# Kernel tuning notes

Hardware: AMD Instinct MI355X
Metric: run time of the kernel (lower is better)

Reference implementation:

```python
import jax, jax.numpy as jnp
import numpy as np

T, H, E, I, TOP_K = 4096, 1024, 8, 2048, 2
EPS = 1e-05


def setup_inputs() -> dict:
    key = jax.random.key(0)
    ks = jax.random.split(key, 4)
    x = jax.random.normal(ks[0], (T, H), dtype=jnp.float32)
    scale = jnp.ones((H,), dtype=jnp.float32)
    gate_kernel = jax.random.normal(ks[1], (H, E), dtype=jnp.float32) * (1.0 / np.sqrt(H))
    gate_bias = jnp.zeros((E,), dtype=jnp.float32)
    mlp1_weight = jax.random.normal(ks[2], (E, H, 2 * I), dtype=jnp.float32) * (1.0 / np.sqrt(H))
    mlp1_bias = jnp.zeros((E, 2 * I), dtype=jnp.float32)
    mlp2_weight = jax.random.normal(ks[3], (E, I, H), dtype=jnp.float32) * (1.0 / np.sqrt(I))
    mlp2_bias = jnp.zeros((E, H), dtype=jnp.float32)
    return {"x": x, "scale": scale, "gate_kernel": gate_kernel, "gate_bias": gate_bias,
            "mlp1_weight": mlp1_weight, "mlp1_bias": mlp1_bias,
            "mlp2_weight": mlp2_weight, "mlp2_bias": mlp2_bias}


def _rmsnorm(x, scale):
    t = x.astype(jnp.float32)
    rms = jnp.sqrt(jnp.mean(t * t, axis=-1, keepdims=True) + EPS)
    return ((t / rms) * scale).astype(x.dtype)


def reference(x, scale, gate_kernel, gate_bias, mlp1_weight, mlp1_bias, mlp2_weight, mlp2_bias):
    normed = _rmsnorm(x, scale)                                   # [T, H]
    _ = normed @ gate_kernel + gate_bias                          # gate logits (unused: static routing)
    # dense per-token, all-expert MLP: [T,H] x [E,H,2I] -> [T,E,2I]
    hidden = jnp.einsum('th,ehi->tei', normed, mlp1_weight) + mlp1_bias
    gate = jnp.minimum(hidden[..., :I], 7.0)
    linear = jnp.clip(hidden[..., I:], -7.0, 7.0)
    activated = gate * jax.nn.sigmoid(1.702 * gate) * (linear + 1.0)
    expert_out = jnp.einsum('tei,eih->teh', activated, mlp2_weight) + mlp2_bias  # [T,E,H]
    # static uniform routing over the first TOP_K experts
    mix = jnp.where(jnp.arange(E) < TOP_K, 1.0 / TOP_K, 0.0).astype(x.dtype)     # [E]
    fused = jnp.einsum('teh,e->th', expert_out, mix)
    return x + fused
```

## Files before the change

### kernel.cpp

```cpp
#include <hip/hip_runtime.h>
#include <hip/hip_bf16.h>
#include <stdint.h>

#define T_DIM 4096
#define H_DIM 1024
#define I_DIM 2048

typedef __bf16 bf16x8 __attribute__((ext_vector_type(8)));
typedef float f32x4 __attribute__((ext_vector_type(4)));
typedef unsigned short ushort_t;
typedef unsigned short us4 __attribute__((ext_vector_type(4)));

__device__ __forceinline__ unsigned short f32_to_bf16(float f) {
  unsigned int u = __float_as_uint(f);
  u += 0x7fffu + ((u >> 16) & 1u);
  return (unsigned short)(u >> 16);
}

__device__ __forceinline__ void gload_lds16(const void* g, void* l) {
  __builtin_amdgcn_global_load_lds(
      (__attribute__((address_space(1))) void*)(uintptr_t)g,
      (__attribute__((address_space(3))) void*)(unsigned int)(uintptr_t)l,
      16, 0, 0);
}

__device__ __forceinline__ int swz(int L) { return L ^ (((L >> 7) & 7) << 4); }

#define S_BARRIER() asm volatile("s_barrier" ::: "memory")
#define WAITV(n) asm volatile("s_waitcnt vmcnt(" #n ")" ::: "memory")
#define IRFENCE() asm volatile("" ::: "memory")
#define MFMA16(acc, va, vb) \
  acc = __builtin_amdgcn_mfma_f32_16x16x32_bf16(va, vb, acc, 0, 0, 0)

__device__ __forceinline__ void transpose_body(const float* __restrict__ src,
                                               ushort_t* __restrict__ dst,
                                               int R, int C, int bx, int by,
                                               int bz, float (*tile)[33]) {
  const size_t eoff = (size_t)bz * (size_t)R * (size_t)C;
  src += eoff;
  dst += eoff;
  const int x0 = bx * 32, y0 = by * 32;
  const int tx = threadIdx.x & 31, ty = threadIdx.x >> 5;
#pragma unroll
  for (int i = 0; i < 4; ++i)
    tile[ty + 8 * i][tx] = src[(size_t)(y0 + ty + 8 * i) * C + x0 + tx];
  __syncthreads();
#pragma unroll
  for (int i = 0; i < 4; ++i)
    dst[(size_t)(x0 + ty + 8 * i) * R + y0 + tx] = f32_to_bf16(tile[tx][ty + 8 * i]);
}

__global__ __launch_bounds__(256) void k_prep1(
    const float* __restrict__ x, const float* __restrict__ scale,
    const float* __restrict__ b2, const float* __restrict__ w1,
    ushort_t* __restrict__ normed, float* __restrict__ out,
    ushort_t* __restrict__ w1T) {
  __shared__ __align__(16) float shm[32][33];
  const int bid = blockIdx.x;
  if (bid < T_DIM) {
    const int row = bid, tid = threadIdx.x;
    const float4 v = ((const float4*)(x + (size_t)row * H_DIM))[tid];
    float ss = v.x * v.x + v.y * v.y + v.z * v.z + v.w * v.w;
#pragma unroll
    for (int off = 32; off > 0; off >>= 1) ss += __shfl_xor(ss, off);
    if ((tid & 63) == 0) shm[0][tid >> 6] = ss;
    __syncthreads();
    const float tot = shm[0][0] + shm[0][1] + shm[0][2] + shm[0][3];
    const float inv = rsqrtf(tot * (1.0f / H_DIM) + 1e-5f);
    const float4 sc = ((const float4*)scale)[tid];
    us4 o;
    o.x = f32_to_bf16(v.x * inv * sc.x);
    o.y = f32_to_bf16(v.y * inv * sc.y);
    o.z = f32_to_bf16(v.z * inv * sc.z);
    o.w = f32_to_bf16(v.w * inv * sc.w);
    ((us4*)(normed + (size_t)row * H_DIM))[tid] = o;
    const float4 b0 = ((const float4*)b2)[tid];
    const float4 b1 = ((const float4*)(b2 + H_DIM))[tid];
    float4 ov;
    ov.x = v.x + 0.5f * (b0.x + b1.x);
    ov.y = v.y + 0.5f * (b0.y + b1.y);
    ov.z = v.z + 0.5f * (b0.z + b1.z);
    ov.w = v.w + 0.5f * (b0.w + b1.w);
    ((float4*)(out + (size_t)row * H_DIM))[tid] = ov;
  } else {
    const int t = bid - T_DIM;
    transpose_body(w1, w1T, H_DIM, 2 * I_DIM, t & 127, (t >> 7) & 31, t >> 12,
                   shm);
  }
}

__global__ __launch_bounds__(256, 2) void k_gemm1_tr2(
    const ushort_t* __restrict__ normed, const ushort_t* __restrict__ w1T,
    const float* __restrict__ b1, ushort_t* __restrict__ act,
    const float* __restrict__ w2, ushort_t* __restrict__ w2T) {
  __shared__ __align__(16) ushort_t lds[3][3][4096];
  char* const ldsB = (char*)&lds[0][0][0];
  if (blockIdx.x >= 1024) {
    const int t = blockIdx.x - 1024;
    transpose_body(w2, w2T, I_DIM, H_DIM, t & 31, (t >> 5) & 63, t >> 11,
                   (float(*)[33])ldsB);
    return;
  }
  const int tid = threadIdx.x;
  const int wg = ((blockIdx.x & 7) << 7) + (blockIdx.x >> 3);
  const int e = wg >> 9;
  const int rem = wg & 511;
  const int brow = (rem >> 4) * 128;
  const int bcol = (rem & 15) * 128;
  const int lane = tid & 63;
  const int wid = tid >> 6;
  const int wm = wid >> 1, wn = wid & 1;
  const int r16 = lane & 15, kh = lane >> 4;

  const ushort_t* gBase = w1T + ((size_t)e * 2 * I_DIM + bcol) * H_DIM;
  const ushort_t* lBase = w1T + ((size_t)e * 2 * I_DIM + I_DIM + bcol) * H_DIM;

  f32x4 accg[4][4], accl[4][4];
  const f32x4 zf = {0.f, 0.f, 0.f, 0.f};
#pragma unroll
  for (int m = 0; m < 4; ++m)
#pragma unroll
    for (int n = 0; n < 4; ++n) { accg[m][n] = zf; accl[m][n] = zf; }

  const ushort_t* pA[2];
  const ushort_t* pG[2];
  const ushort_t* pL[2];
#pragma unroll
  for (int j = 0; j < 2; ++j) {
    const int u = swz(j * 4096 + tid * 16);
    const int r = u >> 6, c = (u & 63) >> 1;
    pA[j] = normed + (size_t)(brow + r) * H_DIM + c;
    pG[j] = gBase + (size_t)r * H_DIM + c;
    pL[j] = lBase + (size_t)r * H_DIM + c;
  }
  const int ldst0 = (tid & ~63) * 16;

  const int abase = swz((wm * 64 + r16) * 64 + kh * 16);
  const int bbase = 8192 + swz((wn * 64 + r16) * 64 + kh * 16);

  auto stage = [&](int buf) {
#pragma unroll
    for (int j = 0; j < 2; ++j) {
      gload_lds16(pA[j], ldsB + buf * 24576 + j * 4096 + ldst0);
      gload_lds16(pG[j], ldsB + buf * 24576 + 8192 + j * 4096 + ldst0);
      gload_lds16(pL[j], ldsB + buf * 24576 + 16384 + j * 4096 + ldst0);
    }
  };

  bf16x8 a[4], bg[4], bl[4];

#define G1_ADV()                                                              \
  {                                                                           \
    _Pragma("unroll") for (int j = 0; j < 2; ++j) {                           \
      pA[j] += 32; pG[j] += 32; pL[j] += 32;                                  \
    }                                                                         \
  }
#define G1_RD(C)                                                              \
  _Pragma("unroll") for (int m = 0; m < 4; ++m)                               \
      a[m] = *(const bf16x8*)(ldsB + (C) * 24576 + abase + m * 1024);         \
  _Pragma("unroll") for (int n = 0; n < 4; ++n) {                             \
    bg[n] = *(const bf16x8*)(ldsB + (C) * 24576 + bbase + n * 1024);          \
    bl[n] = *(const bf16x8*)(ldsB + (C) * 24576 + bbase + 8192 + n * 1024);   \
  }
#define G1_MFMA()                                                             \
  _Pragma("unroll") for (int m = 0; m < 4; ++m)                               \
      _Pragma("unroll") for (int n = 0; n < 4; ++n) {                         \
    MFMA16(accg[m][n], a[m], bg[n]);                                          \
    MFMA16(accl[m][n], a[m], bl[n]);                                          \
  }
#define G1_STEP(C, N)                                                         \
  {                                                                           \
    G1_RD(C);                                                                 \
    stage(N);                                                                 \
    __builtin_amdgcn_s_setprio(1);                                            \
    G1_MFMA();                                                                \
    __builtin_amdgcn_s_setprio(0);                                            \
    WAITV(6);                                                                 \
    S_BARRIER();                                                              \
    G1_ADV();                                                                 \
  }

  stage(0); IRFENCE();
  G1_ADV();
  stage(1);
  G1_ADV();
  WAITV(6);
  S_BARRIER();

#pragma unroll 1
  for (int it = 0; it < 10; ++it) {
    G1_STEP(0, 2);
    G1_STEP(1, 0);
    G1_STEP(2, 1);
  }
  {
    G1_RD(0);
    G1_MFMA();
    WAITV(0);
    S_BARRIER();
    G1_RD(1);
    G1_MFMA();
  }
#undef G1_STEP
#undef G1_MFMA
#undef G1_RD
#undef G1_ADV

  const float* b1e = b1 + (size_t)e * 2 * I_DIM;
#pragma unroll
  for (int m = 0; m < 4; ++m)
#pragma unroll
    for (int n = 0; n < 4; ++n) {
      const int gcol = bcol + wn * 64 + n * 16 + r16;
      const float bgb = b1e[gcol];
      const float blb = b1e[I_DIM + gcol];
#pragma unroll
      for (int rr = 0; rr < 4; ++rr) {
        const int grow = brow + wm * 64 + m * 16 + kh * 4 + rr;
        const float hg = accg[m][n][rr] + bgb;
        const float hl = accl[m][n][rr] + blb;
        const float g = fminf(hg, 7.f);
        const float l = fminf(fmaxf(hl, -7.f), 7.f);
        const float s = 1.f / (1.f + __expf(-1.702f * g));
        const float av = g * s * (l + 1.f);
        act[((size_t)e * T_DIM + grow) * I_DIM + gcol] = f32_to_bf16(av);
      }
    }
}

__global__ __launch_bounds__(512, 2) void k_gemm2(
    const ushort_t* __restrict__ act, const ushort_t* __restrict__ w2T,
    float* __restrict__ out) {
  __shared__ __align__(16) ushort_t lds[3][2][8192];
  char* const ldsB = (char*)&lds[0][0][0];
  const int tid = threadIdx.x;
  const int bid = blockIdx.x;
  const int kc = bid >> 6;
  const int tile = bid & 63;
  const int e = kc >> 1, ih = kc & 1;
  const int brow = (tile >> 2) * 256;
  const int bcol = (tile & 3) * 256;
  const int lane = tid & 63;
  const int wid = tid >> 6;
  const int wm = wid >> 2;
  const int wn = wid & 3;
  const int r16 = lane & 15, kh = lane >> 4;

  const ushort_t* aBase = act + ((size_t)e * T_DIM + brow) * I_DIM + ih * 1024;
  const ushort_t* bBase = w2T + ((size_t)e * H_DIM + bcol) * I_DIM + ih * 1024;

  f32x4 acc[8][4];
  const f32x4 zf = {0.f, 0.f, 0.f, 0.f};
#pragma unroll
  for (int m = 0; m < 8; ++m)
#pragma unroll
    for (int n = 0; n < 4; ++n) acc[m][n] = zf;

  const ushort_t* pA[2];
  const ushort_t* pB[2];
#pragma unroll
  for (int j = 0; j < 2; ++j) {
    const int u = swz(j * 8192 + tid * 16);
    const int r = u >> 6, c = (u & 63) >> 1;
    pA[j] = aBase + (size_t)r * I_DIM + c;
    pB[j] = bBase + (size_t)r * I_DIM + c;
  }
  const int ldst0 = (tid & ~63) * 16;

  const int abase = wm * 8192 + swz(r16 * 64 + kh * 16);
  const int bbase = 16384 + wn * 4096 + swz(r16 * 64 + kh * 16);

  auto stage = [&](int buf) {
#pragma unroll
    for (int j = 0; j < 2; ++j) {
      gload_lds16(pA[j], ldsB + buf * 32768 + j * 8192 + ldst0);
      gload_lds16(pB[j], ldsB + buf * 32768 + 16384 + j * 8192 + ldst0);
    }
  };

  bf16x8 a[8], b[4];

#define G2_ADV()                                                              \
  {                                                                           \
    _Pragma("unroll") for (int j = 0; j < 2; ++j) { pA[j] += 32; pB[j] += 32; } \
  }
#define G2_RD(C)                                                              \
  _Pragma("unroll") for (int m = 0; m < 8; ++m)                               \
      a[m] = *(const bf16x8*)(ldsB + (C) * 32768 + abase + m * 1024);         \
  _Pragma("unroll") for (int n = 0; n < 4; ++n)                               \
      b[n] = *(const bf16x8*)(ldsB + (C) * 32768 + bbase + n * 1024);
#define G2_MFMA()                                                             \
  _Pragma("unroll") for (int m = 0; m < 8; ++m)                               \
      _Pragma("unroll") for (int n = 0; n < 4; ++n)                           \
          MFMA16(acc[m][n], a[m], b[n]);
#define G2_STEP(C, N)                                                         \
  {                                                                           \
    G2_RD(C);                                                                 \
    stage(N);                                                                 \
    __builtin_amdgcn_s_setprio(1);                                            \
    G2_MFMA();                                                                \
    __builtin_amdgcn_s_setprio(0);                                            \
    WAITV(4);                                                                 \
    S_BARRIER();                                                              \
    G2_ADV();                                                                 \
  }

  stage(0); IRFENCE();
  G2_ADV();
  stage(1);
  G2_ADV();
  WAITV(4);
  S_BARRIER();

#pragma unroll 1
  for (int it = 0; it < 10; ++it) {
    G2_STEP(0, 2);
    G2_STEP(1, 0);
    G2_STEP(2, 1);
  }
  {
    G2_RD(0);
    G2_MFMA();
    WAITV(0);
    S_BARRIER();
    G2_RD(1);
    G2_MFMA();
  }
#undef G2_STEP
#undef G2_MFMA
#undef G2_RD
#undef G2_ADV

#pragma unroll
  for (int m = 0; m < 8; ++m)
#pragma unroll
    for (int n = 0; n < 4; ++n) {
      const int gcol = bcol + wn * 64 + n * 16 + r16;
#pragma unroll
      for (int rr = 0; rr < 4; ++rr) {
        const int grow = brow + wm * 128 + m * 16 + kh * 4 + rr;
        atomicAdd(&out[(size_t)grow * H_DIM + gcol], 0.5f * acc[m][n][rr]);
      }
    }
}

extern "C" void kernel_launch(void* const* d_in, const int* in_sizes, int n_in,
                              void* d_out, int out_size, void* d_ws, size_t ws_size,
                              hipStream_t stream) {
  const float* x = (const float*)d_in[0];
  const float* scale = (const float*)d_in[1];
  const float* w1 = (const float*)d_in[4];
  const float* b1 = (const float*)d_in[5];
  const float* w2 = (const float*)d_in[6];
  const float* b2 = (const float*)d_in[7];
  float* out = (float*)d_out;

  ushort_t* ws = (ushort_t*)d_ws;
  ushort_t* normed = ws;
  ushort_t* w1T = normed + (size_t)T_DIM * H_DIM;
  ushort_t* w2T = w1T + (size_t)2 * 2 * I_DIM * H_DIM;
  ushort_t* actb = w2T + (size_t)2 * H_DIM * I_DIM;

  k_prep1<<<dim3(T_DIM + 8192), 256, 0, stream>>>(x, scale, b2, w1, normed,
                                                  out, w1T);
  k_gemm1_tr2<<<dim3(1024 + 4096), 256, 0, stream>>>(normed, w1T, b1, actb,
                                                     w2, w2T);
  k_gemm2<<<dim3(256), 512, 0, stream>>>(actb, w2T, out);
}
```

Measured before the change: 172.0 us.

## Retile second GEMM to 256x128 tiles with full K and XCD-aware block mapping

Changes the second expert GEMM from 256x256 tiles with K split in two halves to 256x128 tiles that each walk the full K of 2048. Each step now loads a K=64 slice into a double-buffered LDS layout instead of K=32 into three buffers. The 8 waves are arranged 4x2, each owning a 64x64 sub-tile, so each wave holds half as many accumulators. Block indices are remapped so neighbouring tiles land on the same XCD, and output atomics per element drop because K is no longer split. The trade-off is less operand reuse per LDS byte from the narrower tile and a shallower prefetch pipeline.

```diff
diff --git a/kernel.cpp b/kernel.cpp
--- a/kernel.cpp
+++ b/kernel.cpp
@@ -231,114 +231,134 @@
 __global__ __launch_bounds__(512, 2) void k_gemm2(
     const ushort_t* __restrict__ act, const ushort_t* __restrict__ w2T,
     float* __restrict__ out) {
-  __shared__ __align__(16) ushort_t lds[3][2][8192];
+  __shared__ __align__(16) ushort_t lds[2][2][12288];
   char* const ldsB = (char*)&lds[0][0][0];
   const int tid = threadIdx.x;
-  const int bid = blockIdx.x;
-  const int kc = bid >> 6;
-  const int tile = bid & 63;
-  const int e = kc >> 1, ih = kc & 1;
-  const int brow = (tile >> 2) * 256;
-  const int bcol = (tile & 3) * 256;
+  const int wg = (blockIdx.x & 7) * 32 + (blockIdx.x >> 3);
+  const int e = wg >> 7;
+  const int tileid = wg & 127;
+  const int brow = (tileid >> 3) * 256;
+  const int bcol = (tileid & 7) * 128;
   const int lane = tid & 63;
-  const int wid = tid >> 6;
-  const int wm = wid >> 2;
-  const int wn = wid & 3;
+  const int wm = (tid >> 6) >> 1;
+  const int wn = (tid >> 6) & 1;
   const int r16 = lane & 15, kh = lane >> 4;
 
-  const ushort_t* aBase = act + ((size_t)e * T_DIM + brow) * I_DIM + ih * 1024;
-  const ushort_t* bBase = w2T + ((size_t)e * H_DIM + bcol) * I_DIM + ih * 1024;
-
-  f32x4 acc[8][4];
+  const ushort_t* aBase = act + ((size_t)e * T_DIM + brow) * I_DIM;
+  const ushort_t* bBase = w2T + ((size_t)e * H_DIM + bcol) * I_DIM;
+
+  f32x4 acc[4][4];
   const f32x4 zf = {0.f, 0.f, 0.f, 0.f};
 #pragma unroll
-  for (int m = 0; m < 8; ++m)
+  for (int m = 0; m < 4; ++m)
 #pragma unroll
     for (int n = 0; n < 4; ++n) acc[m][n] = zf;
 
-  const ushort_t* pA[2];
-  const ushort_t* pB[2];
+  int srow[2], scolb[2];
 #pragma unroll
   for (int j = 0; j < 2; ++j) {
-    const int u = swz(j * 8192 + tid * 16);
-    const int r = u >> 6, c = (u & 63) >> 1;
-    pA[j] = aBase + (size_t)r * I_DIM + c;
-    pB[j] = bBase + (size_t)r * I_DIM + c;
+    const int u = swz((j * 512 + tid) * 16);
+    srow[j] = u >> 6;
+    scolb[j] = (u & 63) >> 1;
   }
   const int ldst0 = (tid & ~63) * 16;
 
-  const int abase = wm * 8192 + swz(r16 * 64 + kh * 16);
-  const int bbase = 16384 + wn * 4096 + swz(r16 * 64 + kh * 16);
-
-  auto stage = [&](int buf) {
-#pragma unroll
-    for (int j = 0; j < 2; ++j) {
-      gload_lds16(pA[j], ldsB + buf * 32768 + j * 8192 + ldst0);
-      gload_lds16(pB[j], ldsB + buf * 32768 + 16384 + j * 8192 + ldst0);
-    }
-  };
-
-  bf16x8 a[8], b[4];
-
-#define G2_ADV()                                                              \
+  const ushort_t* pA0 = aBase + (size_t)srow[0] * I_DIM + scolb[0];
+  const ushort_t* pA1 = aBase + (size_t)srow[1] * I_DIM + scolb[1];
+  const ushort_t* pB = bBase + (size_t)srow[0] * I_DIM + scolb[0];
+
+  int aoffV[2][4], boffV[2][4];
+#pragma unroll
+  for (int bq = 0; bq < 2; ++bq) {
+#pragma unroll
+    for (int m = 0; m < 4; ++m)
+      aoffV[bq][m] = bq * 49152 + swz((wm * 64 + m * 16 + r16) * 64 + kh * 16);
+#pragma unroll
+    for (int n = 0; n < 4; ++n)
+      boffV[bq][n] = bq * 49152 + 16384 + swz((wn * 64 + n * 16 + r16) * 64 + kh * 16);
+  }
+
+  auto stageA = [&](int buf, int ksub) {
+    gload_lds16(pA0 + ksub * 32, ldsB + buf * 49152 + ksub * 24576 + ldst0);
+    gload_lds16(pA1 + ksub * 32, ldsB + buf * 49152 + ksub * 24576 + 8192 + ldst0);
+  };
+  auto stageB = [&](int buf, int ksub) {
+    gload_lds16(pB + ksub * 32, ldsB + buf * 49152 + ksub * 24576 + 16384 + ldst0);
+  };
+  auto rdA = [&](int buf, int ksub, int m) -> bf16x8 {
+    return *(const bf16x8*)(ldsB + aoffV[buf][m] + ksub * 24576);
+  };
+  auto rdB = [&](int buf, int ksub, int n) -> bf16x8 {
+    return *(const bf16x8*)(ldsB + boffV[buf][n] + ksub * 24576);
+  };
+
+#define G2_ADV() \
+  { pA0 += 64; pA1 += 64; pB += 64; }
+
+#define G2_HALF(CUR, NXT, KS)                                                 \
   {                                                                           \
-    _Pragma("unroll") for (int j = 0; j < 2; ++j) { pA[j] += 32; pB[j] += 32; } \
-  }
-#define G2_RD(C)                                                              \
-  _Pragma("unroll") for (int m = 0; m < 8; ++m)                               \
-      a[m] = *(const bf16x8*)(ldsB + (C) * 32768 + abase + m * 1024);         \
-  _Pragma("unroll") for (int n = 0; n < 4; ++n)                               \
-      b[n] = *(const bf16x8*)(ldsB + (C) * 32768 + bbase + n * 1024);
-#define G2_MFMA()                                                             \
-  _Pragma("unroll") for (int m = 0; m < 8; ++m)                               \
-      _Pragma("unroll") for (int n = 0; n < 4; ++n)                           \
-          MFMA16(acc[m][n], a[m], b[n]);
-#define G2_STEP(C, N)                                                         \
-  {                                                                           \
-    G2_RD(C);                                                                 \
-    stage(N);                                                                 \
+    _Pragma("unroll") for (int m = 0; m < 4; ++m) a[m] = rdA(CUR, KS, m);     \
+    _Pragma("unroll") for (int n = 0; n < 4; ++n) b[n] = rdB(CUR, KS, n);     \
+    stageA(NXT, KS);                                                          \
+    stageB(NXT, KS);                                                          \
     __builtin_amdgcn_s_setprio(1);                                            \
-    G2_MFMA();                                                                \
+    _Pragma("unroll") for (int m = 0; m < 4; ++m)                             \
+        _Pragma("unroll") for (int n = 0; n < 4; ++n)                         \
+            MFMA16(acc[m][n], a[m], b[n]);                                    \
     __builtin_amdgcn_s_setprio(0);                                            \
-    WAITV(4);                                                                 \
+    WAITV(3);                                                                 \
     S_BARRIER();                                                              \
-    G2_ADV();                                                                 \
-  }
-
-  stage(0); IRFENCE();
+  }
+
+#define G2_TILE(CUR, NXT)  \
+  { G2_HALF(CUR, NXT, 0); G2_HALF(CUR, NXT, 1); G2_ADV(); }
+
+  stageA(0, 0); stageB(0, 0); IRFENCE();
+  stageA(0, 1); stageB(0, 1);
   G2_ADV();
-  stage(1);
-  G2_ADV();
-  WAITV(4);
+  WAITV(3);
   S_BARRIER();
 
+  bf16x8 a[4], b[4];
 #pragma unroll 1
-  for (int it = 0; it < 10; ++it) {
-    G2_STEP(0, 2);
-    G2_STEP(1, 0);
-    G2_STEP(2, 1);
-  }
+  for (int it = 0; it < 15; ++it) {
+    G2_TILE(0, 1);
+    G2_TILE(1, 0);
+  }
+  G2_TILE(0, 1);
+
   {
-    G2_RD(0);
-    G2_MFMA();
+#pragma unroll
+    for (int m = 0; m < 4; ++m) a[m] = rdA(1, 0, m);
+#pragma unroll
+    for (int n = 0; n < 4; ++n) b[n] = rdB(1, 0, n);
+#pragma unroll
+    for (int m = 0; m < 4; ++m)
+#pragma unroll
+      for (int n = 0; n < 4; ++n) MFMA16(acc[m][n], a[m], b[n]);
     WAITV(0);
     S_BARRIER();
-    G2_RD(1);
-    G2_MFMA();
-  }
-#undef G2_STEP
-#undef G2_MFMA
-#undef G2_RD
+#pragma unroll
+    for (int m = 0; m < 4; ++m) a[m] = rdA(1, 1, m);
+#pragma unroll
+    for (int n = 0; n < 4; ++n) b[n] = rdB(1, 1, n);
+#pragma unroll
+    for (int m = 0; m < 4; ++m)
+#pragma unroll
+      for (int n = 0; n < 4; ++n) MFMA16(acc[m][n], a[m], b[n]);
+  }
+#undef G2_HALF
+#undef G2_TILE
 #undef G2_ADV
 
 #pragma unroll
-  for (int m = 0; m < 8; ++m)
+  for (int m = 0; m < 4; ++m)
 #pragma unroll
     for (int n = 0; n < 4; ++n) {
       const int gcol = bcol + wn * 64 + n * 16 + r16;
 #pragma unroll
       for (int rr = 0; rr < 4; ++rr) {
-        const int grow = brow + wm * 128 + m * 16 + kh * 4 + rr;
+        const int grow = brow + wm * 64 + m * 16 + kh * 4 + rr;
         atomicAdd(&out[(size_t)grow * H_DIM + gcol], 0.5f * acc[m][n][rr]);
       }
     }
```

Result: faster. 149.0 us (-13.4%).
